# Kernel tuning notes

Measured on AMD Instinct MI355X. Metric: run time of the kernel, lower is better.

## Reference

```python
import jax, jax.numpy as jnp
import numpy as np

B, T, D_EMBED, HEAD = 8, 4096, 128, 64


def setup_inputs() -> dict:
    key = jax.random.key(0)
    k1, k2, k3, k4 = jax.random.split(key, 4)
    x = jax.random.normal(k1, (B, T, D_EMBED), dtype=jnp.float32)
    # torch nn.Linear(d_embed, head_size, bias=False): y = x @ W^T, W:[head,in].
    # We store W already transposed as [in, head] for x @ W.
    Wq = jax.random.normal(k2, (D_EMBED, HEAD), dtype=jnp.float32) * (1.0 / np.sqrt(D_EMBED))
    Wk = jax.random.normal(k3, (D_EMBED, HEAD), dtype=jnp.float32) * (1.0 / np.sqrt(D_EMBED))
    Wv = jax.random.normal(k4, (D_EMBED, HEAD), dtype=jnp.float32) * (1.0 / np.sqrt(D_EMBED))
    return {"x": x, "Wq": Wq, "Wk": Wk, "Wv": Wv}


def reference(x, Wq, Wk, Wv):
    # x: [B, T, D]; projections to [B, T, H]
    T_ = x.shape[1]
    D_ = x.shape[2]
    Q = x @ Wq
    K = x @ Wk
    V = x @ Wv
    # NOTE: source divides by sqrt(feature_dimension) == sqrt(d_embed), not head_size
    scores = jnp.einsum('bqh,bkh->bqk', Q, K) / jnp.sqrt(jnp.float32(D_))
    causal = jnp.tril(jnp.ones((T_, T_), dtype=bool))  # [T, T]
    scores = jnp.where(causal[None, :, :], scores, -jnp.inf)
    probs = jax.nn.softmax(scores, axis=-1)  # [B, T, T]
    return jnp.einsum('bqk,bkh->bqh', probs, V)
```

## Files before the change

### kernel.cpp

```cpp
#include <hip/hip_runtime.h>
#include <hip/hip_bf16.h>

typedef __attribute__((ext_vector_type(8))) short bf16x8;
typedef __attribute__((ext_vector_type(4))) short short4v;
typedef __attribute__((ext_vector_type(4))) float f32x4;

#define MFMA16(a, b, c) __builtin_amdgcn_mfma_f32_16x16x32_bf16((a), (b), (c), 0, 0, 0)

constexpr int Bn = 8, Tn = 4096, Dn = 128, Hn = 64;

__device__ inline unsigned short f2b(float f) {
    union { float f; unsigned u; } v; v.f = f;
    unsigned r = v.u + 0x7fff + ((v.u >> 16) & 1);
    return (unsigned short)(r >> 16);
}

__global__ void wtrans(const float* __restrict__ Wq,
                       const float* __restrict__ Wk,
                       const float* __restrict__ Wv,
                       unsigned short* __restrict__ WT) {
    int m = blockIdx.x;
    const float* W = (m == 0) ? Wq : (m == 1) ? Wk : Wv;
    unsigned short* o = WT + m * Hn * Dn;
    for (int i = threadIdx.x; i < Hn * Dn; i += blockDim.x) {
        int n = i >> 7, k = i & 127;
        o[i] = f2b(W[k * Hn + n]);
    }
}

__global__ __launch_bounds__(256) void qkv(const float* __restrict__ X,
                                           const unsigned short* __restrict__ WT,
                                           unsigned short* __restrict__ Qp,
                                           unsigned short* __restrict__ Kp,
                                           unsigned short* __restrict__ VTp) {
    __shared__ unsigned short xt[64 * 136];
    __shared__ unsigned short ot[64 * 72];
    int tid = threadIdx.x, w = tid >> 6, lane = tid & 63, quad = lane >> 4, l15 = lane & 15;
    int m0 = blockIdx.x * 64;
    int b = m0 >> 12, tloc = m0 & (Tn - 1);

    #pragma unroll
    for (int c = 0; c < 8; c++) {
        int e = tid * 4 + c * 1024;
        int row = e >> 7, col = e & 127;
        f32x4 v = *(const f32x4*)&X[(size_t)(m0 + row) * Dn + col];
        short4v s4;
        s4[0] = (short)f2b(v[0]); s4[1] = (short)f2b(v[1]);
        s4[2] = (short)f2b(v[2]); s4[3] = (short)f2b(v[3]);
        *(short4v*)&xt[row * 136 + col] = s4;
    }
    __syncthreads();

    bf16x8 a[4];
    #pragma unroll
    for (int kt = 0; kt < 4; kt++)
        a[kt] = *(const bf16x8*)&xt[(w * 16 + l15) * 136 + kt * 32 + quad * 8];

    for (int mat = 0; mat < 3; mat++) {
        f32x4 acc[4];
        #pragma unroll
        for (int nt = 0; nt < 4; nt++) {
            acc[nt] = (f32x4){0.f, 0.f, 0.f, 0.f};
            const unsigned short* wtm = WT + mat * Hn * Dn + (size_t)(nt * 16 + l15) * Dn + quad * 8;
            #pragma unroll
            for (int kt = 0; kt < 4; kt++)
                acc[nt] = MFMA16(a[kt], *(const bf16x8*)&wtm[kt * 32], acc[nt]);
        }
        __syncthreads();
        if (mat < 2) {
            #pragma unroll
            for (int nt = 0; nt < 4; nt++)
                #pragma unroll
                for (int rg = 0; rg < 4; rg++)
                    ot[(w * 16 + quad * 4 + rg) * 72 + nt * 16 + l15] = f2b(acc[nt][rg]);
        } else {
            #pragma unroll
            for (int nt = 0; nt < 4; nt++) {
                short4v pk;
                pk[0] = (short)f2b(acc[nt][0]); pk[1] = (short)f2b(acc[nt][1]);
                pk[2] = (short)f2b(acc[nt][2]); pk[3] = (short)f2b(acc[nt][3]);
                *(short4v*)&ot[(nt * 16 + l15) * 72 + w * 16 + quad * 4] = pk;
            }
        }
        __syncthreads();
        if (mat < 2) {
            unsigned short* O = mat ? Kp : Qp;
            #pragma unroll
            for (int i = 0; i < 2; i++) {
                int row = (tid >> 3) + 32 * i, ch = tid & 7;
                *(bf16x8*)&O[(size_t)(m0 + row) * Hn + ch * 8] = *(const bf16x8*)&ot[row * 72 + ch * 8];
            }
        } else {
            #pragma unroll
            for (int i = 0; i < 2; i++) {
                int h = (tid >> 3) + 32 * i, ch = tid & 7;
                *(bf16x8*)&VTp[((size_t)(b * Hn + h)) * Tn + tloc + ch * 8] = *(const bf16x8*)&ot[h * 72 + ch * 8];
            }
        }
    }
}

__global__ __launch_bounds__(256) void attn(const unsigned short* __restrict__ Qp,
                                            const unsigned short* __restrict__ Kp,
                                            const unsigned short* __restrict__ VTp,
                                            float* __restrict__ Out) {
    __shared__ unsigned short Ps[4][32 * 40];
    __shared__ float Cbuf[2][32][66];
    __shared__ float Lbuf[2][64];

    int idx = blockIdx.x;
    int b = idx & 7;
    int j = (idx >> 3) & 31;
    int qt = (idx >> 8) ? j : (63 - j);

    int tid = threadIdx.x, w = tid >> 6, lane = tid & 63, quad = lane >> 4, l15 = lane & 15;
    int qh = w & 1, kh = w >> 1;
    const float kLog2Scale = 0.12751879523175464f;

    int Q0 = qt * 64;
    const unsigned short* Kb = Kp + (size_t)b * Tn * Hn;
    const unsigned short* Vb = VTp + (size_t)b * Hn * Tn;

    bf16x8 qf[2][2];
    {
        const unsigned short* Qb = Qp + ((size_t)b * Tn + Q0 + qh * 32) * Hn;
        #pragma unroll
        for (int nq = 0; nq < 2; nq++)
            #pragma unroll
            for (int hc = 0; hc < 2; hc++)
                qf[nq][hc] = *(const bf16x8*)&Qb[(nq * 16 + l15) * Hn + hc * 32 + quad * 8];
    }

    f32x4 o[2][4];
    #pragma unroll
    for (int nq = 0; nq < 2; nq++)
        #pragma unroll
        for (int nh = 0; nh < 4; nh++) o[nq][nh] = (f32x4){0.f, 0.f, 0.f, 0.f};
    float li[2] = {0.f, 0.f};

    unsigned short* Pw = &Ps[w][0];

    for (int kt = 0; kt <= qt; kt++) {
        int kk = kt * 64 + kh * 32;
        bf16x8 kf[2][2];
        #pragma unroll
        for (int mt = 0; mt < 2; mt++)
            #pragma unroll
            for (int hc = 0; hc < 2; hc++)
                kf[mt][hc] = *(const bf16x8*)&Kb[(size_t)(kk + mt * 16 + l15) * Hn + hc * 32 + quad * 8];
        bf16x8 vf[4];
        #pragma unroll
        for (int nh = 0; nh < 4; nh++)
            vf[nh] = *(const bf16x8*)&Vb[(size_t)(nh * 16 + l15) * Tn + kk + quad * 8];

        f32x4 s[2][2];
        #pragma unroll
        for (int mt = 0; mt < 2; mt++)
            #pragma unroll
            for (int nq = 0; nq < 2; nq++) {
                f32x4 acc = {0.f, 0.f, 0.f, 0.f};
                acc = MFMA16(kf[mt][0], qf[nq][0], acc);
                acc = MFMA16(kf[mt][1], qf[nq][1], acc);
                s[mt][nq] = acc;
            }

        bool diag = (kt == qt);
        int kbase = kk + quad * 4;
        int qbase = Q0 + qh * 32 + l15;
        #pragma unroll
        for (int mt = 0; mt < 2; mt++) {
            #pragma unroll
            for (int nq = 0; nq < 2; nq++) {
                short4v pk;
                #pragma unroll
                for (int rg = 0; rg < 4; rg++) {
                    float p = __builtin_amdgcn_exp2f(s[mt][nq][rg] * kLog2Scale);
                    if (diag && (kbase + mt * 16 + rg > qbase + nq * 16)) p = 0.f;
                    li[nq] += p;
                    pk[rg] = (short)f2b(p);
                }
                *(short4v*)&Pw[(nq * 16 + l15) * 40 + mt * 16 + quad * 4] = pk;
            }
        }
        bf16x8 pf[2];
        #pragma unroll
        for (int nq = 0; nq < 2; nq++)
            pf[nq] = *(const bf16x8*)&Pw[(nq * 16 + l15) * 40 + quad * 8];
        #pragma unroll
        for (int nq = 0; nq < 2; nq++)
            #pragma unroll
            for (int nh = 0; nh < 4; nh++)
                o[nq][nh] = MFMA16(pf[nq], vf[nh], o[nq][nh]);
    }

    __syncthreads();
    #pragma unroll
    for (int nq = 0; nq < 2; nq++) {
        li[nq] += __shfl_xor(li[nq], 16);
        li[nq] += __shfl_xor(li[nq], 32);
    }
    if (lane < 16) {
        Lbuf[kh][qh * 32 + lane]      = li[0];
        Lbuf[kh][qh * 32 + 16 + lane] = li[1];
    }
    if (kh == 1) {
        #pragma unroll
        for (int nq = 0; nq < 2; nq++)
            #pragma unroll
            for (int nh = 0; nh < 4; nh++)
                #pragma unroll
                for (int rg = 0; rg < 4; rg++)
                    Cbuf[qh][nq * 16 + quad * 4 + rg][nh * 16 + l15] = o[nq][nh][rg];
    }
    __syncthreads();
    if (kh == 0) {
        #pragma unroll
        for (int nq = 0; nq < 2; nq++) {
            #pragma unroll
            for (int rg = 0; rg < 4; rg++) {
                int qloc = nq * 16 + quad * 4 + rg;
                float lt = Lbuf[0][qh * 32 + qloc] + Lbuf[1][qh * 32 + qloc];
                float inv = 1.0f / lt;
                size_t row = (size_t)b * Tn + Q0 + qh * 32 + qloc;
                #pragma unroll
                for (int nh = 0; nh < 4; nh++) {
                    float val = o[nq][nh][rg] + Cbuf[qh][qloc][nh * 16 + l15];
                    Out[row * Hn + nh * 16 + l15] = val * inv;
                }
            }
        }
    }
}

extern "C" void kernel_launch(void* const* d_in, const int* in_sizes, int n_in,
                              void* d_out, int out_size, void* d_ws, size_t ws_size,
                              hipStream_t stream) {
    const float* X  = (const float*)d_in[0];
    const float* Wq = (const float*)d_in[1];
    const float* Wk = (const float*)d_in[2];
    const float* Wv = (const float*)d_in[3];
    float* out = (float*)d_out;

    char* ws = (char*)d_ws;
    size_t szQ = (size_t)Bn * Tn * Hn * sizeof(unsigned short);
    unsigned short* Qp  = (unsigned short*)(ws);
    unsigned short* Kp  = (unsigned short*)(ws + szQ);
    unsigned short* VTp = (unsigned short*)(ws + 2 * szQ);
    unsigned short* WT  = (unsigned short*)(ws + 3 * szQ);

    wtrans<<<3, 256, 0, stream>>>(Wq, Wk, Wv, WT);
    qkv<<<Bn * Tn / 64, 256, 0, stream>>>(X, WT, Qp, Kp, VTp);
    attn<<<Bn * Tn / 64, 256, 0, stream>>>(Qp, Kp, VTp, out);
}
```

Before: 153.9 us.

## Double-buffer K/V register loads and fold softmax scale into Q projection

The attention loop now prefetches the next K and V fragments into a second register set while it computes on the current ones, ping-ponging between two buffers. This hides global-load latency behind the MFMA and exp work. The log2 softmax scale is also applied to Q when the projection kernel writes it out, which removes one multiply per score. Holding two sets of fragments raises register pressure, and rounding the pre-scaled Q to bf16 changes numerics slightly.

```diff
diff --git a/kernel.cpp b/kernel.cpp
--- a/kernel.cpp
+++ b/kernel.cpp
@@ -38,6 +38,7 @@
     int tid = threadIdx.x, w = tid >> 6, lane = tid & 63, quad = lane >> 4, l15 = lane & 15;
     int m0 = blockIdx.x * 64;
     int b = m0 >> 12, tloc = m0 & (Tn - 1);
+    const float kLog2Scale = 0.12751879523175464f;
 
     #pragma unroll
     for (int c = 0; c < 8; c++) {
@@ -68,11 +69,12 @@
         }
         __syncthreads();
         if (mat < 2) {
+            float sc = (mat == 0) ? kLog2Scale : 1.0f;
             #pragma unroll
             for (int nt = 0; nt < 4; nt++)
                 #pragma unroll
                 for (int rg = 0; rg < 4; rg++)
-                    ot[(w * 16 + quad * 4 + rg) * 72 + nt * 16 + l15] = f2b(acc[nt][rg]);
+                    ot[(w * 16 + quad * 4 + rg) * 72 + nt * 16 + l15] = f2b(acc[nt][rg] * sc);
         } else {
             #pragma unroll
             for (int nt = 0; nt < 4; nt++) {
@@ -115,12 +117,31 @@
 
     int tid = threadIdx.x, w = tid >> 6, lane = tid & 63, quad = lane >> 4, l15 = lane & 15;
     int qh = w & 1, kh = w >> 1;
-    const float kLog2Scale = 0.12751879523175464f;
 
     int Q0 = qt * 64;
     const unsigned short* Kb = Kp + (size_t)b * Tn * Hn;
     const unsigned short* Vb = VTp + (size_t)b * Hn * Tn;
 
+    f32x4 o[2][4];
+    #pragma unroll
+    for (int nq = 0; nq < 2; nq++)
+        #pragma unroll
+        for (int nh = 0; nh < 4; nh++) o[nq][nh] = (f32x4){0.f, 0.f, 0.f, 0.f};
+    float li[2] = {0.f, 0.f};
+    unsigned short* Pw = &Ps[w][0];
+
+    bf16x8 kf0[2][2], vf0[4], kf1[2][2], vf1[4];
+    {
+        int kk = kh * 32;
+        #pragma unroll
+        for (int mt = 0; mt < 2; mt++)
+            #pragma unroll
+            for (int hc = 0; hc < 2; hc++)
+                kf0[mt][hc] = *(const bf16x8*)&Kb[(size_t)(kk + mt * 16 + l15) * Hn + hc * 32 + quad * 8];
+        #pragma unroll
+        for (int nh = 0; nh < 4; nh++)
+            vf0[nh] = *(const bf16x8*)&Vb[(size_t)(nh * 16 + l15) * Tn + kk + quad * 8];
+    }
     bf16x8 qf[2][2];
     {
         const unsigned short* Qb = Qp + ((size_t)b * Tn + Q0 + qh * 32) * Hn;
@@ -131,39 +152,30 @@
                 qf[nq][hc] = *(const bf16x8*)&Qb[(nq * 16 + l15) * Hn + hc * 32 + quad * 8];
     }
 
-    f32x4 o[2][4];
-    #pragma unroll
-    for (int nq = 0; nq < 2; nq++)
-        #pragma unroll
-        for (int nh = 0; nh < 4; nh++) o[nq][nh] = (f32x4){0.f, 0.f, 0.f, 0.f};
-    float li[2] = {0.f, 0.f};
-
-    unsigned short* Pw = &Ps[w][0];
-
-    for (int kt = 0; kt <= qt; kt++) {
+    auto body = [&](bf16x8 (&kc)[2][2], bf16x8 (&vc)[4],
+                    bf16x8 (&kn)[2][2], bf16x8 (&vn)[4], int kt) {
+        if (kt < qt) {
+            int kk2 = (kt + 1) * 64 + kh * 32;
+            #pragma unroll
+            for (int mt = 0; mt < 2; mt++)
+                #pragma unroll
+                for (int hc = 0; hc < 2; hc++)
+                    kn[mt][hc] = *(const bf16x8*)&Kb[(size_t)(kk2 + mt * 16 + l15) * Hn + hc * 32 + quad * 8];
+            #pragma unroll
+            for (int nh = 0; nh < 4; nh++)
+                vn[nh] = *(const bf16x8*)&Vb[(size_t)(nh * 16 + l15) * Tn + kk2 + quad * 8];
+        }
         int kk = kt * 64 + kh * 32;
-        bf16x8 kf[2][2];
-        #pragma unroll
-        for (int mt = 0; mt < 2; mt++)
-            #pragma unroll
-            for (int hc = 0; hc < 2; hc++)
-                kf[mt][hc] = *(const bf16x8*)&Kb[(size_t)(kk + mt * 16 + l15) * Hn + hc * 32 + quad * 8];
-        bf16x8 vf[4];
-        #pragma unroll
-        for (int nh = 0; nh < 4; nh++)
-            vf[nh] = *(const bf16x8*)&Vb[(size_t)(nh * 16 + l15) * Tn + kk + quad * 8];
-
         f32x4 s[2][2];
         #pragma unroll
         for (int mt = 0; mt < 2; mt++)
             #pragma unroll
             for (int nq = 0; nq < 2; nq++) {
                 f32x4 acc = {0.f, 0.f, 0.f, 0.f};
-                acc = MFMA16(kf[mt][0], qf[nq][0], acc);
-                acc = MFMA16(kf[mt][1], qf[nq][1], acc);
+                acc = MFMA16(kc[mt][0], qf[nq][0], acc);
+                acc = MFMA16(kc[mt][1], qf[nq][1], acc);
                 s[mt][nq] = acc;
             }
-
         bool diag = (kt == qt);
         int kbase = kk + quad * 4;
         int qbase = Q0 + qh * 32 + l15;
@@ -174,7 +186,7 @@
                 short4v pk;
                 #pragma unroll
                 for (int rg = 0; rg < 4; rg++) {
-                    float p = __builtin_amdgcn_exp2f(s[mt][nq][rg] * kLog2Scale);
+                    float p = __builtin_amdgcn_exp2f(s[mt][nq][rg]);
                     if (diag && (kbase + mt * 16 + rg > qbase + nq * 16)) p = 0.f;
                     li[nq] += p;
                     pk[rg] = (short)f2b(p);
@@ -190,7 +202,15 @@
         for (int nq = 0; nq < 2; nq++)
             #pragma unroll
             for (int nh = 0; nh < 4; nh++)
-                o[nq][nh] = MFMA16(pf[nq], vf[nh], o[nq][nh]);
+                o[nq][nh] = MFMA16(pf[nq], vc[nh], o[nq][nh]);
+    };
+
+    int kt = 0;
+    for (;;) {
+        body(kf0, vf0, kf1, vf1, kt);
+        if (++kt > qt) break;
+        body(kf1, vf1, kf0, vf0, kt);
+        if (++kt > qt) break;
     }
 
     __syncthreads();
```

Measured after the change: 153.1 us. No clear change (-0.5%).

## Stage K/V tiles in shared memory with register prefetch, fold scale into Q

Applied to the files above, without the earlier changes.

The attention kernel now uses 128-thread blocks, each covering 32 query rows. The block cooperatively loads each 64-key K/V tile into LDS, prefetching the next tile into registers while computing the current one, so warps no longer each read K/V from global memory. The softmax scale (log2e/sqrt(D)) is folded into Q during projection, which removes a multiply per score. Scheduling becomes a plain descending query-tile order. The trade-offs are extra barriers per tile and halved work per block, and rounding the scaled Q to bf16 slightly shifts numerics.

```diff
diff --git a/kernel.cpp b/kernel.cpp
--- a/kernel.cpp
+++ b/kernel.cpp
@@ -38,6 +38,7 @@
     int tid = threadIdx.x, w = tid >> 6, lane = tid & 63, quad = lane >> 4, l15 = lane & 15;
     int m0 = blockIdx.x * 64;
     int b = m0 >> 12, tloc = m0 & (Tn - 1);
+    const float kLog2Scale = 0.12751879523175464f;
 
     #pragma unroll
     for (int c = 0; c < 8; c++) {
@@ -68,11 +69,12 @@
         }
         __syncthreads();
         if (mat < 2) {
+            float sc = (mat == 0) ? kLog2Scale : 1.0f;
             #pragma unroll
             for (int nt = 0; nt < 4; nt++)
                 #pragma unroll
                 for (int rg = 0; rg < 4; rg++)
-                    ot[(w * 16 + quad * 4 + rg) * 72 + nt * 16 + l15] = f2b(acc[nt][rg]);
+                    ot[(w * 16 + quad * 4 + rg) * 72 + nt * 16 + l15] = f2b(acc[nt][rg] * sc);
         } else {
             #pragma unroll
             for (int nt = 0; nt < 4; nt++) {
@@ -100,27 +102,36 @@
     }
 }
 
-__global__ __launch_bounds__(256) void attn(const unsigned short* __restrict__ Qp,
+__global__ __launch_bounds__(128) void attn(const unsigned short* __restrict__ Qp,
                                             const unsigned short* __restrict__ Kp,
                                             const unsigned short* __restrict__ VTp,
                                             float* __restrict__ Out) {
-    __shared__ unsigned short Ps[4][32 * 40];
-    __shared__ float Cbuf[2][32][66];
-    __shared__ float Lbuf[2][64];
+    __shared__ unsigned short Ks[64 * 72];
+    __shared__ unsigned short Vs[64 * 72];
+    __shared__ unsigned short Ps[2][32 * 40];
+    __shared__ float Cbuf[32][66];
+    __shared__ float Lbuf[2][32];
 
     int idx = blockIdx.x;
     int b = idx & 7;
-    int j = (idx >> 3) & 31;
-    int qt = (idx >> 8) ? j : (63 - j);
+    int qh = (idx >> 3) & 1;
+    int qt = 63 - (idx >> 4);
 
     int tid = threadIdx.x, w = tid >> 6, lane = tid & 63, quad = lane >> 4, l15 = lane & 15;
-    int qh = w & 1, kh = w >> 1;
-    const float kLog2Scale = 0.12751879523175464f;
-
+    int kh = w;
     int Q0 = qt * 64;
     const unsigned short* Kb = Kp + (size_t)b * Tn * Hn;
     const unsigned short* Vb = VTp + (size_t)b * Hn * Tn;
 
+    int srow = tid >> 3, scol = (tid & 7) * 8;
+    const f32x4* Ksrc = (const f32x4*)Kb;
+
+    f32x4 kr[4], vr[4];
+    #pragma unroll
+    for (int i = 0; i < 4; i++) kr[i] = Ksrc[tid + i * 128];
+    #pragma unroll
+    for (int i = 0; i < 4; i++) vr[i] = *(const f32x4*)&Vb[(size_t)(srow + i * 16) * Tn + scol];
+
     bf16x8 qf[2][2];
     {
         const unsigned short* Qb = Qp + ((size_t)b * Tn + Q0 + qh * 32) * Hn;
@@ -137,21 +148,32 @@
         #pragma unroll
         for (int nh = 0; nh < 4; nh++) o[nq][nh] = (f32x4){0.f, 0.f, 0.f, 0.f};
     float li[2] = {0.f, 0.f};
-
     unsigned short* Pw = &Ps[w][0];
 
     for (int kt = 0; kt <= qt; kt++) {
-        int kk = kt * 64 + kh * 32;
-        bf16x8 kf[2][2];
+        __syncthreads();
+        #pragma unroll
+        for (int i = 0; i < 4; i++) *(f32x4*)&Ks[(srow + i * 16) * 72 + scol] = kr[i];
+        #pragma unroll
+        for (int i = 0; i < 4; i++) *(f32x4*)&Vs[(srow + i * 16) * 72 + scol] = vr[i];
+        __syncthreads();
+        if (kt < qt) {
+            #pragma unroll
+            for (int i = 0; i < 4; i++) kr[i] = Ksrc[(kt + 1) * 512 + tid + i * 128];
+            #pragma unroll
+            for (int i = 0; i < 4; i++)
+                vr[i] = *(const f32x4*)&Vb[(size_t)(srow + i * 16) * Tn + (kt + 1) * 64 + scol];
+        }
+
+        bf16x8 kf[2][2], vf[4];
         #pragma unroll
         for (int mt = 0; mt < 2; mt++)
             #pragma unroll
             for (int hc = 0; hc < 2; hc++)
-                kf[mt][hc] = *(const bf16x8*)&Kb[(size_t)(kk + mt * 16 + l15) * Hn + hc * 32 + quad * 8];
-        bf16x8 vf[4];
+                kf[mt][hc] = *(const bf16x8*)&Ks[(kh * 32 + mt * 16 + l15) * 72 + hc * 32 + quad * 8];
         #pragma unroll
         for (int nh = 0; nh < 4; nh++)
-            vf[nh] = *(const bf16x8*)&Vb[(size_t)(nh * 16 + l15) * Tn + kk + quad * 8];
+            vf[nh] = *(const bf16x8*)&Vs[(nh * 16 + l15) * 72 + kh * 32 + quad * 8];
 
         f32x4 s[2][2];
         #pragma unroll
@@ -165,7 +187,7 @@
             }
 
         bool diag = (kt == qt);
-        int kbase = kk + quad * 4;
+        int kbase = kt * 64 + kh * 32 + quad * 4;
         int qbase = Q0 + qh * 32 + l15;
         #pragma unroll
         for (int mt = 0; mt < 2; mt++) {
@@ -174,7 +196,7 @@
                 short4v pk;
                 #pragma unroll
                 for (int rg = 0; rg < 4; rg++) {
-                    float p = __builtin_amdgcn_exp2f(s[mt][nq][rg] * kLog2Scale);
+                    float p = __builtin_amdgcn_exp2f(s[mt][nq][rg]);
                     if (diag && (kbase + mt * 16 + rg > qbase + nq * 16)) p = 0.f;
                     li[nq] += p;
                     pk[rg] = (short)f2b(p);
@@ -200,31 +222,31 @@
         li[nq] += __shfl_xor(li[nq], 32);
     }
     if (lane < 16) {
-        Lbuf[kh][qh * 32 + lane]      = li[0];
-        Lbuf[kh][qh * 32 + 16 + lane] = li[1];
-    }
-    if (kh == 1) {
+        Lbuf[w][lane]      = li[0];
+        Lbuf[w][16 + lane] = li[1];
+    }
+    if (w == 1) {
         #pragma unroll
         for (int nq = 0; nq < 2; nq++)
             #pragma unroll
             for (int nh = 0; nh < 4; nh++)
                 #pragma unroll
                 for (int rg = 0; rg < 4; rg++)
-                    Cbuf[qh][nq * 16 + quad * 4 + rg][nh * 16 + l15] = o[nq][nh][rg];
+                    Cbuf[nq * 16 + quad * 4 + rg][nh * 16 + l15] = o[nq][nh][rg];
     }
     __syncthreads();
-    if (kh == 0) {
+    if (w == 0) {
         #pragma unroll
         for (int nq = 0; nq < 2; nq++) {
             #pragma unroll
             for (int rg = 0; rg < 4; rg++) {
                 int qloc = nq * 16 + quad * 4 + rg;
-                float lt = Lbuf[0][qh * 32 + qloc] + Lbuf[1][qh * 32 + qloc];
+                float lt = Lbuf[0][qloc] + Lbuf[1][qloc];
                 float inv = 1.0f / lt;
                 size_t row = (size_t)b * Tn + Q0 + qh * 32 + qloc;
                 #pragma unroll
                 for (int nh = 0; nh < 4; nh++) {
-                    float val = o[nq][nh][rg] + Cbuf[qh][qloc][nh * 16 + l15];
+                    float val = o[nq][nh][rg] + Cbuf[qloc][nh * 16 + l15];
                     Out[row * Hn + nh * 16 + l15] = val * inv;
                 }
             }
@@ -250,5 +272,5 @@
 
     wtrans<<<3, 256, 0, stream>>>(Wq, Wk, Wv, WT);
     qkv<<<Bn * Tn / 64, 256, 0, stream>>>(X, WT, Qp, Kp, VTp);
-    attn<<<Bn * Tn / 64, 256, 0, stream>>>(Qp, Kp, VTp, out);
-}
+    attn<<<1024, 128, 0, stream>>>(Qp, Kp, VTp, out);
+}
```

Result: faster. 150.8 us (-2.0%).

## Split long causal query tiles across key chunks and combine partials in fuse kernel

Applied to the files above, without the earlier changes.

The attention kernel now splits query tiles with many key tiles into up to four 16-tile key chunks, giving 1280 blocks of more even work instead of 512 unbalanced ones. Partial numerators go to bf16 workspace and row sums to a separate buffer, and a new fuse kernel adds them and normalises. K and V tiles are staged through shared memory with a register prefetch of the next tile, and the softmax scale is folded into Q during projection. This costs an extra launch, partial-result traffic and bf16 rounding of the partials, and adds more block barriers per iteration.

```diff
diff --git a/kernel.cpp b/kernel.cpp
--- a/kernel.cpp
+++ b/kernel.cpp
@@ -13,6 +13,10 @@
     union { float f; unsigned u; } v; v.f = f;
     unsigned r = v.u + 0x7fff + ((v.u >> 16) & 1);
     return (unsigned short)(r >> 16);
+}
+__device__ inline float b2f(unsigned short u) {
+    union { unsigned u; float f; } v; v.u = ((unsigned)u) << 16;
+    return v.f;
 }
 
 __global__ void wtrans(const float* __restrict__ Wq,
@@ -38,6 +42,7 @@
     int tid = threadIdx.x, w = tid >> 6, lane = tid & 63, quad = lane >> 4, l15 = lane & 15;
     int m0 = blockIdx.x * 64;
     int b = m0 >> 12, tloc = m0 & (Tn - 1);
+    const float kLog2Scale = 0.12751879523175464f;
 
     #pragma unroll
     for (int c = 0; c < 8; c++) {
@@ -68,11 +73,12 @@
         }
         __syncthreads();
         if (mat < 2) {
+            float sc = (mat == 0) ? kLog2Scale : 1.0f;
             #pragma unroll
             for (int nt = 0; nt < 4; nt++)
                 #pragma unroll
                 for (int rg = 0; rg < 4; rg++)
-                    ot[(w * 16 + quad * 4 + rg) * 72 + nt * 16 + l15] = f2b(acc[nt][rg]);
+                    ot[(w * 16 + quad * 4 + rg) * 72 + nt * 16 + l15] = f2b(acc[nt][rg] * sc);
         } else {
             #pragma unroll
             for (int nt = 0; nt < 4; nt++) {
@@ -103,24 +109,40 @@
 __global__ __launch_bounds__(256) void attn(const unsigned short* __restrict__ Qp,
                                             const unsigned short* __restrict__ Kp,
                                             const unsigned short* __restrict__ VTp,
-                                            float* __restrict__ Out) {
-    __shared__ unsigned short Ps[4][32 * 40];
-    __shared__ float Cbuf[2][32][66];
+                                            float* __restrict__ Out,
+                                            unsigned short* __restrict__ Part,
+                                            float* __restrict__ Lpart) {
+    __shared__ __align__(16) char shmem[18432];
+    unsigned short* Ks = (unsigned short*)shmem;
+    unsigned short* Vs = Ks + 64 * 72;
+    __shared__ __align__(16) unsigned short Ps[4][32 * 40];
     __shared__ float Lbuf[2][64];
 
     int idx = blockIdx.x;
     int b = idx & 7;
-    int j = (idx >> 3) & 31;
-    int qt = (idx >> 8) ? j : (63 - j);
+    int c = 159 - (idx >> 3);
+    int qt, ch, nch;
+    if (c < 16)      { qt = c;                 ch = 0;          nch = 1; }
+    else if (c < 48) { int t = c - 16; qt = 16 + (t >> 1); ch = t & 1;      nch = 2; }
+    else if (c < 96) { int t = c - 48; int q3 = t / 3; qt = 32 + q3; ch = t - 3 * q3; nch = 3; }
+    else             { int t = c - 96; qt = 48 + (t >> 2); ch = t & 3;      nch = 4; }
+    int k0 = ch * 16, k1 = min(qt, k0 + 15);
 
     int tid = threadIdx.x, w = tid >> 6, lane = tid & 63, quad = lane >> 4, l15 = lane & 15;
     int qh = w & 1, kh = w >> 1;
-    const float kLog2Scale = 0.12751879523175464f;
-
     int Q0 = qt * 64;
     const unsigned short* Kb = Kp + (size_t)b * Tn * Hn;
     const unsigned short* Vb = VTp + (size_t)b * Hn * Tn;
 
+    int srow = tid >> 3, scol = (tid & 7) * 8;
+    const f32x4* Ksrc = (const f32x4*)Kb;
+
+    f32x4 kr[2], vr[2];
+    #pragma unroll
+    for (int i = 0; i < 2; i++) kr[i] = Ksrc[k0 * 512 + tid + i * 256];
+    #pragma unroll
+    for (int i = 0; i < 2; i++) vr[i] = *(const f32x4*)&Vb[(size_t)(srow + i * 32) * Tn + k0 * 64 + scol];
+
     bf16x8 qf[2][2];
     {
         const unsigned short* Qb = Qp + ((size_t)b * Tn + Q0 + qh * 32) * Hn;
@@ -137,21 +159,32 @@
         #pragma unroll
         for (int nh = 0; nh < 4; nh++) o[nq][nh] = (f32x4){0.f, 0.f, 0.f, 0.f};
     float li[2] = {0.f, 0.f};
-
     unsigned short* Pw = &Ps[w][0];
 
-    for (int kt = 0; kt <= qt; kt++) {
-        int kk = kt * 64 + kh * 32;
-        bf16x8 kf[2][2];
+    for (int kt = k0; kt <= k1; kt++) {
+        __syncthreads();
+        #pragma unroll
+        for (int i = 0; i < 2; i++) *(f32x4*)&Ks[(srow + i * 32) * 72 + scol] = kr[i];
+        #pragma unroll
+        for (int i = 0; i < 2; i++) *(f32x4*)&Vs[(srow + i * 32) * 72 + scol] = vr[i];
+        __syncthreads();
+        if (kt < k1) {
+            #pragma unroll
+            for (int i = 0; i < 2; i++) kr[i] = Ksrc[(kt + 1) * 512 + tid + i * 256];
+            #pragma unroll
+            for (int i = 0; i < 2; i++)
+                vr[i] = *(const f32x4*)&Vb[(size_t)(srow + i * 32) * Tn + (kt + 1) * 64 + scol];
+        }
+
+        bf16x8 kf[2][2], vf[4];
         #pragma unroll
         for (int mt = 0; mt < 2; mt++)
             #pragma unroll
             for (int hc = 0; hc < 2; hc++)
-                kf[mt][hc] = *(const bf16x8*)&Kb[(size_t)(kk + mt * 16 + l15) * Hn + hc * 32 + quad * 8];
-        bf16x8 vf[4];
+                kf[mt][hc] = *(const bf16x8*)&Ks[(kh * 32 + mt * 16 + l15) * 72 + hc * 32 + quad * 8];
         #pragma unroll
         for (int nh = 0; nh < 4; nh++)
-            vf[nh] = *(const bf16x8*)&Vb[(size_t)(nh * 16 + l15) * Tn + kk + quad * 8];
+            vf[nh] = *(const bf16x8*)&Vs[(nh * 16 + l15) * 72 + kh * 32 + quad * 8];
 
         f32x4 s[2][2];
         #pragma unroll
@@ -165,7 +198,7 @@
             }
 
         bool diag = (kt == qt);
-        int kbase = kk + quad * 4;
+        int kbase = kt * 64 + kh * 32 + quad * 4;
         int qbase = Q0 + qh * 32 + l15;
         #pragma unroll
         for (int mt = 0; mt < 2; mt++) {
@@ -174,7 +207,7 @@
                 short4v pk;
                 #pragma unroll
                 for (int rg = 0; rg < 4; rg++) {
-                    float p = __builtin_amdgcn_exp2f(s[mt][nq][rg] * kLog2Scale);
+                    float p = __builtin_amdgcn_exp2f(s[mt][nq][rg]);
                     if (diag && (kbase + mt * 16 + rg > qbase + nq * 16)) p = 0.f;
                     li[nq] += p;
                     pk[rg] = (short)f2b(p);
@@ -194,6 +227,7 @@
     }
 
     __syncthreads();
+    float (*Cbuf)[32][66] = (float (*)[32][66])shmem;
     #pragma unroll
     for (int nq = 0; nq < 2; nq++) {
         li[nq] += __shfl_xor(li[nq], 16);
@@ -214,21 +248,65 @@
     }
     __syncthreads();
     if (kh == 0) {
+        if (nch > 1 && lane < 32)
+            Lpart[(((size_t)b * 64 + qt) * 4 + ch) * 64 + qh * 32 + lane] =
+                Lbuf[0][qh * 32 + lane] + Lbuf[1][qh * 32 + lane];
+        int slot = b * 96 + ((qt < 32) ? (qt - 16)
+                   : (qt < 48) ? 16 + 2 * (qt - 32) + (ch - 1)
+                               : 48 + 3 * (qt - 48) + (ch - 1));
         #pragma unroll
         for (int nq = 0; nq < 2; nq++) {
             #pragma unroll
             for (int rg = 0; rg < 4; rg++) {
                 int qloc = nq * 16 + quad * 4 + rg;
                 float lt = Lbuf[0][qh * 32 + qloc] + Lbuf[1][qh * 32 + qloc];
-                float inv = 1.0f / lt;
                 size_t row = (size_t)b * Tn + Q0 + qh * 32 + qloc;
-                #pragma unroll
-                for (int nh = 0; nh < 4; nh++) {
-                    float val = o[nq][nh][rg] + Cbuf[qh][qloc][nh * 16 + l15];
-                    Out[row * Hn + nh * 16 + l15] = val * inv;
+                if (nch == 1) {
+                    float inv = 1.0f / lt;
+                    #pragma unroll
+                    for (int nh = 0; nh < 4; nh++)
+                        Out[row * Hn + nh * 16 + l15] =
+                            (o[nq][nh][rg] + Cbuf[qh][qloc][nh * 16 + l15]) * inv;
+                } else if (ch == 0) {
+                    #pragma unroll
+                    for (int nh = 0; nh < 4; nh++)
+                        Out[row * Hn + nh * 16 + l15] =
+                            o[nq][nh][rg] + Cbuf[qh][qloc][nh * 16 + l15];
+                } else {
+                    #pragma unroll
+                    for (int nh = 0; nh < 4; nh++)
+                        Part[(size_t)slot * 4096 + (qh * 32 + qloc) * 64 + nh * 16 + l15] =
+                            f2b(o[nq][nh][rg] + Cbuf[qh][qloc][nh * 16 + l15]);
                 }
             }
         }
+    }
+}
+
+__global__ __launch_bounds__(256) void fuse(float* __restrict__ Out,
+                                            const unsigned short* __restrict__ Part,
+                                            const float* __restrict__ Lpart) {
+    int blk = blockIdx.x;
+    int b = blk / 48, qt = 16 + blk % 48;
+    int nch = (qt < 32) ? 2 : (qt < 48) ? 3 : 4;
+    int tid = threadIdx.x;
+    size_t gbase = ((size_t)b * Tn + qt * 64) * Hn;
+    const float* Lp = &Lpart[((size_t)b * 64 + qt) * 4 * 64];
+
+    #pragma unroll 4
+    for (int i = 0; i < 16; i++) {
+        int e = tid + i * 256;
+        int q = e >> 6;
+        float L = 0.f;
+        for (int cc = 0; cc < nch; cc++) L += Lp[cc * 64 + q];
+        float val = Out[gbase + e];
+        for (int cc = 1; cc < nch; cc++) {
+            int slot = b * 96 + ((qt < 32) ? (qt - 16)
+                       : (qt < 48) ? 16 + 2 * (qt - 32) + (cc - 1)
+                                   : 48 + 3 * (qt - 48) + (cc - 1));
+            val += b2f(Part[(size_t)slot * 4096 + e]);
+        }
+        Out[gbase + e] = val / L;
     }
 }
 
@@ -247,8 +325,11 @@
     unsigned short* Kp  = (unsigned short*)(ws + szQ);
     unsigned short* VTp = (unsigned short*)(ws + 2 * szQ);
     unsigned short* WT  = (unsigned short*)(ws + 3 * szQ);
+    float*          Lp  = (float*)(ws + 3 * szQ + (64 << 10));
+    unsigned short* Pt  = (unsigned short*)(ws + 3 * szQ + (64 << 10) + (512 << 10));
 
     wtrans<<<3, 256, 0, stream>>>(Wq, Wk, Wv, WT);
     qkv<<<Bn * Tn / 64, 256, 0, stream>>>(X, WT, Qp, Kp, VTp);
-    attn<<<Bn * Tn / 64, 256, 0, stream>>>(Qp, Kp, VTp, out);
-}
+    attn<<<1280, 256, 0, stream>>>(Qp, Kp, VTp, out, Pt, Lp);
+    fuse<<<8 * 48, 256, 0, stream>>>(out, Pt, Lp);
+}
```

Result: slower. 164.8 us (+7.0%).
